# Performance work log

Measured on AMD Instinct MI355X. Metric: run time of the kernel, lower is better.

Reference implementation:

```python
import jax, jax.numpy as jnp
import numpy as np

CHUNKS = 4      # number of segments along in_features
QMAX = 127.0    # int8 symmetric fake quantization
EPS = 1e-8


def fake_quantize(t):
    """Per-tensor symmetric int8 fake quantization with amax scaling (STE-friendly)."""
    amax = jnp.max(jnp.abs(t))
    scale = jnp.maximum(amax / QMAX, EPS)
    q = jnp.clip(jnp.round(t / scale), -QMAX, QMAX) * scale
    # straight-through estimator: identity gradient through the quantizer
    return t + jax.lax.stop_gradient(q - t)


def setup_inputs() -> dict:
    key = jax.random.key(0)
    kx, kw = jax.random.split(key)
    N, K, O = 4096, 4096, 4096  # tokens (B*S), in_features, out_features
    x = jax.random.normal(kx, (N, K), dtype=jnp.float32)
    weight = jax.random.normal(kw, (O, K), dtype=jnp.float32)
    return {"x": x, "weight": weight}


def reference(x, weight):
    # seg_mode='input': split x and weight along in_features into CHUNKS equal chunks,
    # fake-quantize each chunk independently (per-chunk amax scale), run per-chunk
    # GEMMs y_i = fq(x_i) @ fq(w_i)^T and sum over chunks. No bias in 'input' mode.
    N, K = x.shape
    O = weight.shape[0]
    cs = K // CHUNKS
    xc = x.reshape(N, CHUNKS, cs)       # [N, C, cs]
    wc = weight.reshape(O, CHUNKS, cs)  # [O, C, cs]
    fq_chunks = jax.vmap(fake_quantize, in_axes=1, out_axes=1)  # independent amax per chunk
    xq = fq_chunks(xc)
    wq = fq_chunks(wc)
    # sum of per-chunk matmuls == contraction over (chunk, within-chunk) axes
    return jnp.einsum('nck,ock->no', xq, wq)
```

## Files before the change

kernel.cpp:

```cpp
#include <hip/hip_runtime.h>
#include <hip/hip_bf16.h>


constexpr int NDIM = 4096;
constexpr int TOTAL4 = (NDIM * NDIM) / 4;

typedef int i32x4 __attribute__((ext_vector_type(4)));

__global__ __launch_bounds__(256) void amax_kernel(
    const float* __restrict__ x, const float* __restrict__ w,
    unsigned int* __restrict__ amax) {
  const int t = threadIdx.x;
  const int c = blockIdx.x & 3;
  float mx = 0.f, mw = 0.f;
  const float4* x4 = (const float4*)x;
  const float4* w4 = (const float4*)w;
  const int stride = 1024 * 256;
  for (int i = blockIdx.x * 256 + t; i < TOTAL4; i += stride) {
    float4 v = x4[i];
    mx = fmaxf(mx, fmaxf(fmaxf(fabsf(v.x), fabsf(v.y)),
                         fmaxf(fabsf(v.z), fabsf(v.w))));
    float4 u = w4[i];
    mw = fmaxf(mw, fmaxf(fmaxf(fabsf(u.x), fabsf(u.y)),
                         fmaxf(fabsf(u.z), fabsf(u.w))));
  }
  __shared__ float r0[256], r1[256];
  r0[t] = mx; r1[t] = mw;
  __syncthreads();
  for (int off = 128; off; off >>= 1) {
    if (t < off) {
      r0[t] = fmaxf(r0[t], r0[t + off]);
      r1[t] = fmaxf(r1[t], r1[t + off]);
    }
    __syncthreads();
  }
  if (t == 0) {
    atomicMax(&amax[c],     __float_as_uint(r0[0]));
    atomicMax(&amax[4 + c], __float_as_uint(r1[0]));
  }
}

__device__ __forceinline__ signed char quant1(float v, float s) {
  float r = rintf(v / s);
  r = fminf(fmaxf(r, -127.f), 127.f);
  return (signed char)(int)r;
}

__global__ __launch_bounds__(256) void quant_kernel(
    const float* __restrict__ x, const float* __restrict__ w,
    const unsigned int* __restrict__ amax,
    signed char* __restrict__ qx, signed char* __restrict__ qw) {
  const int t = threadIdx.x;
  const int c = blockIdx.x & 3;
  const float sx = fmaxf(__uint_as_float(amax[c])     / 127.0f, 1e-8f);
  const float sw = fmaxf(__uint_as_float(amax[4 + c]) / 127.0f, 1e-8f);
  const float4* x4 = (const float4*)x;
  const float4* w4 = (const float4*)w;
  char4* qx4 = (char4*)qx;
  char4* qw4 = (char4*)qw;
  const int stride = 1024 * 256;
  for (int i = blockIdx.x * 256 + t; i < TOTAL4; i += stride) {
    float4 v = x4[i];
    char4 q;
    q.x = quant1(v.x, sx); q.y = quant1(v.y, sx);
    q.z = quant1(v.z, sx); q.w = quant1(v.w, sx);
    qx4[i] = q;
    float4 u = w4[i];
    char4 p;
    p.x = quant1(u.x, sw); p.y = quant1(u.y, sw);
    p.z = quant1(u.z, sw); p.w = quant1(u.w, sw);
    qw4[i] = p;
  }
}

__device__ __forceinline__ void async16(const void* g, void* l) {
  __builtin_amdgcn_global_load_lds(
      (const __attribute__((address_space(1))) void*)g,
      (__attribute__((address_space(3))) void*)l, 16, 0, 0);
}

__global__ __launch_bounds__(256, 2) void gemm_i8_kernel(
    const signed char* __restrict__ qx, const signed char* __restrict__ qw,
    const unsigned int* __restrict__ amax, float* __restrict__ out) {
  __shared__ __align__(1024) signed char lds_a[2][16384];
  __shared__ __align__(1024) signed char lds_b[2][16384];

  const int t = threadIdx.x;
  const int lane = t & 63;
  const int wave = t >> 6;
  const int brow = blockIdx.y * 128;
  const int bcol = blockIdx.x * 128;
  const int wr = wave >> 1;
  const int wc = wave & 1;

  const float s0 = fmaxf(__uint_as_float(amax[0]) / 127.0f, 1e-8f) *
                   fmaxf(__uint_as_float(amax[4]) / 127.0f, 1e-8f);
  const float s1 = fmaxf(__uint_as_float(amax[1]) / 127.0f, 1e-8f) *
                   fmaxf(__uint_as_float(amax[5]) / 127.0f, 1e-8f);
  const float s2 = fmaxf(__uint_as_float(amax[2]) / 127.0f, 1e-8f) *
                   fmaxf(__uint_as_float(amax[6]) / 127.0f, 1e-8f);
  const float s3 = fmaxf(__uint_as_float(amax[3]) / 127.0f, 1e-8f) *
                   fmaxf(__uint_as_float(amax[7]) / 127.0f, 1e-8f);
  asm volatile("s_waitcnt vmcnt(0)" ::: "memory");
  __builtin_amdgcn_sched_barrier(0);

  const int srow = t >> 3;
  const int scol = (((t & 7) ^ (srow & 7)) << 4);
  const signed char* gA = qx + (size_t)(brow + srow) * NDIM + scol;
  const signed char* gB = qw + (size_t)(bcol + srow) * NDIM + scol;
  signed char* laW = &lds_a[0][0] + wave * 1024;
  signed char* lbW = &lds_b[0][0] + wave * 1024;

  const int kg = lane >> 4;
  const int l7 = lane & 7;
  const int sk0 = ((kg) ^ l7) << 4;
  const int sk1 = ((4 + kg) ^ l7) << 4;
  const int rba = (wr * 64 + (lane & 15)) * 128;
  const int rbb = (wc * 64 + (lane & 15)) * 128;

#define STAGE(BUFOFF, T)                                              \
  do {                                                                \
    const size_t kt_ = (size_t)(T) * 128;                             \
    async16(gA + kt_,                  laW + (BUFOFF));               \
    async16(gA + kt_ + 32u * NDIM,     laW + (BUFOFF) + 4096);        \
    async16(gA + kt_ + 64u * NDIM,     laW + (BUFOFF) + 8192);        \
    async16(gA + kt_ + 96u * NDIM,     laW + (BUFOFF) + 12288);       \
    async16(gB + kt_,                  lbW + (BUFOFF));               \
    async16(gB + kt_ + 32u * NDIM,     lbW + (BUFOFF) + 4096);        \
    async16(gB + kt_ + 64u * NDIM,     lbW + (BUFOFF) + 8192);        \
    async16(gB + kt_ + 96u * NDIM,     lbW + (BUFOFF) + 12288);       \
  } while (0)

  STAGE(0, 0);
  STAGE(16384, 1);

  i32x4 iacc[4][4];
  float facc[4][4][4];
#pragma unroll
  for (int m = 0; m < 4; ++m)
#pragma unroll
    for (int n = 0; n < 4; ++n) {
      iacc[m][n] = i32x4{0, 0, 0, 0};
#pragma unroll
      for (int j = 0; j < 4; ++j) facc[m][n][j] = 0.f;
    }

#define HALF(LA, LB, SK)                                                \
  do {                                                                  \
    i32x4 av[4], bv[4];                                                 \
    _Pragma("unroll")                                                   \
    for (int m = 0; m < 4; ++m)                                         \
      av[m] = *(const i32x4*)&(LA)[rba + m * 2048 + (SK)];              \
    _Pragma("unroll")                                                   \
    for (int n = 0; n < 4; ++n)                                         \
      bv[n] = *(const i32x4*)&(LB)[rbb + n * 2048 + (SK)];              \
    __builtin_amdgcn_s_setprio(1);                                      \
    _Pragma("unroll")                                                   \
    for (int m = 0; m < 4; ++m)                                         \
      _Pragma("unroll")                                                 \
      for (int n = 0; n < 4; ++n)                                       \
        iacc[m][n] = __builtin_amdgcn_mfma_i32_16x16x64_i8(             \
            av[m], bv[n], iacc[m][n], 0, 0, 0);                         \
    __builtin_amdgcn_s_setprio(0);                                      \
  } while (0)

#define COMPUTE(BUFOFF)                                                 \
  do {                                                                  \
    const signed char* la_ = &lds_a[0][0] + (BUFOFF);                   \
    const signed char* lb_ = &lds_b[0][0] + (BUFOFF);                   \
    HALF(la_, lb_, sk0);                                                \
    HALF(la_, lb_, sk1);                                                \
  } while (0)

#define FOLD(S)                                                         \
  do {                                                                  \
    _Pragma("unroll")                                                   \
    for (int m = 0; m < 4; ++m)                                         \
      _Pragma("unroll")                                                 \
      for (int n = 0; n < 4; ++n) {                                     \
        _Pragma("unroll")                                               \
        for (int j = 0; j < 4; ++j) facc[m][n][j] += (S) * (float)iacc[m][n][j]; \
        iacc[m][n] = i32x4{0, 0, 0, 0};                                 \
      }                                                                 \
  } while (0)

#define WAITV(N) \
  asm volatile("s_waitcnt vmcnt(" #N ")" ::: "memory"); \
  __builtin_amdgcn_sched_barrier(0)
#define WAITL \
  asm volatile("s_waitcnt lgkmcnt(0)" ::: "memory"); \
  __builtin_amdgcn_sched_barrier(0)
#define BAR \
  __builtin_amdgcn_s_barrier(); \
  __builtin_amdgcn_sched_barrier(0)

#pragma unroll 1
  for (int it = 0; it < 15; ++it) {
    WAITV(8); BAR;
    COMPUTE(0);
    WAITL; BAR;
    STAGE(0, 2 * it + 2);
    WAITV(8); BAR;
    COMPUTE(16384);
    WAITL; BAR;
    STAGE(16384, 2 * it + 3);
    if ((it & 3) == 3) {
      const int ci = it >> 2;
      FOLD(ci == 0 ? s0 : ci == 1 ? s1 : s2);
    }
  }
  WAITV(8); BAR;
  COMPUTE(0);
  WAITL; BAR;
  WAITV(0); BAR;
  COMPUTE(16384);
  FOLD(s3);

  const int orow = brow + wr * 64 + (lane >> 4) * 4;
  const int ocol = bcol + wc * 64 + (lane & 15);
#pragma unroll
  for (int m = 0; m < 4; ++m)
#pragma unroll
    for (int n = 0; n < 4; ++n)
#pragma unroll
      for (int j = 0; j < 4; ++j)
        out[(size_t)(orow + m * 16 + j) * NDIM + (ocol + n * 16)] = facc[m][n][j];
#undef STAGE
#undef HALF
#undef COMPUTE
#undef FOLD
#undef WAITV
#undef WAITL
#undef BAR
}

extern "C" void kernel_launch(void* const* d_in, const int* in_sizes, int n_in,
                              void* d_out, int out_size, void* d_ws, size_t ws_size,
                              hipStream_t stream) {
  const float* x = (const float*)d_in[0];
  const float* w = (const float*)d_in[1];
  float* out = (float*)d_out;

  unsigned int* amax = (unsigned int*)d_ws;
  signed char* qx = (signed char*)d_ws + 256;
  signed char* qw = qx + (size_t)NDIM * NDIM;

  hipMemsetAsync(d_ws, 0, 256, stream);
  amax_kernel<<<1024, 256, 0, stream>>>(x, w, amax);
  quant_kernel<<<1024, 256, 0, stream>>>(x, w, amax, qx, qw);
  dim3 grid(NDIM / 128, NDIM / 128);
  gemm_i8_kernel<<<grid, 256, 0, stream>>>(qx, qw, amax, out);
}
```

Measured before the change: 144.9 us.

## Load A operand directly to registers and 4-stage B pipeline in LDS

The int8 GEMM stops staging the A tile through LDS. Each wave now loads its A fragments straight from global memory into registers, double-buffered across K steps. The B tile moves to a 4-buffer LDS ring with one barrier per K step instead of two. Occupancy drops to one block per CU, and A rows are no longer shared between the two waves that use them, which doubles A global traffic and raises register pressure.

```diff
diff --git a/kernel.cpp b/kernel.cpp
--- a/kernel.cpp
+++ b/kernel.cpp
@@ -79,11 +79,10 @@
       (__attribute__((address_space(3))) void*)l, 16, 0, 0);
 }
 
-__global__ __launch_bounds__(256, 2) void gemm_i8_kernel(
+__global__ __launch_bounds__(256, 1) void gemm_i8_kernel(
     const signed char* __restrict__ qx, const signed char* __restrict__ qw,
     const unsigned int* __restrict__ amax, float* __restrict__ out) {
-  __shared__ __align__(1024) signed char lds_a[2][16384];
-  __shared__ __align__(1024) signed char lds_b[2][16384];
+  __shared__ __align__(1024) signed char lds_b[4][16384];
 
   const int t = threadIdx.x;
   const int lane = t & 63;
@@ -101,39 +100,54 @@
                    fmaxf(__uint_as_float(amax[6]) / 127.0f, 1e-8f);
   const float s3 = fmaxf(__uint_as_float(amax[3]) / 127.0f, 1e-8f) *
                    fmaxf(__uint_as_float(amax[7]) / 127.0f, 1e-8f);
-  asm volatile("s_waitcnt vmcnt(0)" ::: "memory");
+  asm volatile("s_waitcnt vmcnt(0) lgkmcnt(0)" ::: "memory");
   __builtin_amdgcn_sched_barrier(0);
 
   const int srow = t >> 3;
   const int scol = (((t & 7) ^ (srow & 7)) << 4);
-  const signed char* gA = qx + (size_t)(brow + srow) * NDIM + scol;
   const signed char* gB = qw + (size_t)(bcol + srow) * NDIM + scol;
-  signed char* laW = &lds_a[0][0] + wave * 1024;
-  signed char* lbW = &lds_b[0][0] + wave * 1024;
-
+
+  const int l15 = lane & 15;
   const int kg = lane >> 4;
+  const signed char* gA = qx + (size_t)(brow + wr * 64 + l15) * NDIM + kg * 16;
+
   const int l7 = lane & 7;
   const int sk0 = ((kg) ^ l7) << 4;
   const int sk1 = ((4 + kg) ^ l7) << 4;
-  const int rba = (wr * 64 + (lane & 15)) * 128;
-  const int rbb = (wc * 64 + (lane & 15)) * 128;
-
-#define STAGE(BUFOFF, T)                                              \
+  const int rbb = (wc * 64 + l15) * 128;
+
+#define STAGE_B(BUF, T)                                               \
   do {                                                                \
     const size_t kt_ = (size_t)(T) * 128;                             \
-    async16(gA + kt_,                  laW + (BUFOFF));               \
-    async16(gA + kt_ + 32u * NDIM,     laW + (BUFOFF) + 4096);        \
-    async16(gA + kt_ + 64u * NDIM,     laW + (BUFOFF) + 8192);        \
-    async16(gA + kt_ + 96u * NDIM,     laW + (BUFOFF) + 12288);       \
-    async16(gB + kt_,                  lbW + (BUFOFF));               \
-    async16(gB + kt_ + 32u * NDIM,     lbW + (BUFOFF) + 4096);        \
-    async16(gB + kt_ + 64u * NDIM,     lbW + (BUFOFF) + 8192);        \
-    async16(gB + kt_ + 96u * NDIM,     lbW + (BUFOFF) + 12288);       \
-  } while (0)
-
-  STAGE(0, 0);
-  STAGE(16384, 1);
-
+    async16(gB + kt_,              &lds_b[BUF][0] + t * 16);          \
+    async16(gB + kt_ + 32u * NDIM, &lds_b[BUF][4096] + t * 16);       \
+    async16(gB + kt_ + 64u * NDIM, &lds_b[BUF][8192] + t * 16);       \
+    async16(gB + kt_ + 96u * NDIM, &lds_b[BUF][12288] + t * 16);      \
+  } while (0)
+
+#define LOAD_A(SET, T)                                                \
+  do {                                                                \
+    const size_t kt_ = (size_t)(T) * 128;                             \
+    _Pragma("unroll")                                                 \
+    for (int m = 0; m < 4; ++m)                                       \
+      _Pragma("unroll")                                               \
+      for (int h = 0; h < 2; ++h)                                     \
+        SET[m][h] = *(const i32x4*)(gA + kt_ +                        \
+                                    (size_t)m * (16u * NDIM) + h * 64); \
+  } while (0)
+
+#define MM(AV, BV, M, N) \
+  iacc[M][N] = __builtin_amdgcn_mfma_i32_16x16x64_i8((AV), (BV), iacc[M][N], 0, 0, 0)
+
+#define SCB  __builtin_amdgcn_sched_barrier(0)
+#define WAITV(N) \
+  asm volatile("s_waitcnt vmcnt(" #N ")" ::: "memory"); SCB
+#define WAITL \
+  asm volatile("s_waitcnt lgkmcnt(0)" ::: "memory"); SCB
+#define BAR \
+  __builtin_amdgcn_s_barrier(); SCB
+
+  i32x4 aA[4][2], aB[4][2];
   i32x4 iacc[4][4];
   float facc[4][4][4];
 #pragma unroll
@@ -145,31 +159,27 @@
       for (int j = 0; j < 4; ++j) facc[m][n][j] = 0.f;
     }
 
-#define HALF(LA, LB, SK)                                                \
+  STAGE_B(0, 0); SCB;
+  LOAD_A(aA, 0); SCB;
+  STAGE_B(1, 1); SCB;
+
+#define COMPUTE(BUF, SET)                                               \
   do {                                                                  \
-    i32x4 av[4], bv[4];                                                 \
+    i32x4 bv[4][2];                                                     \
     _Pragma("unroll")                                                   \
-    for (int m = 0; m < 4; ++m)                                         \
-      av[m] = *(const i32x4*)&(LA)[rba + m * 2048 + (SK)];              \
-    _Pragma("unroll")                                                   \
-    for (int n = 0; n < 4; ++n)                                         \
-      bv[n] = *(const i32x4*)&(LB)[rbb + n * 2048 + (SK)];              \
+    for (int n = 0; n < 4; ++n) {                                       \
+      bv[n][0] = *(const i32x4*)&lds_b[BUF][rbb + n * 2048 + sk0];      \
+      bv[n][1] = *(const i32x4*)&lds_b[BUF][rbb + n * 2048 + sk1];      \
+    }                                                                   \
     __builtin_amdgcn_s_setprio(1);                                      \
     _Pragma("unroll")                                                   \
-    for (int m = 0; m < 4; ++m)                                         \
+    for (int h = 0; h < 2; ++h)                                         \
       _Pragma("unroll")                                                 \
-      for (int n = 0; n < 4; ++n)                                       \
-        iacc[m][n] = __builtin_amdgcn_mfma_i32_16x16x64_i8(             \
-            av[m], bv[n], iacc[m][n], 0, 0, 0);                         \
+      for (int m = 0; m < 4; ++m)                                       \
+        _Pragma("unroll")                                               \
+        for (int n = 0; n < 4; ++n)                                     \
+          MM(SET[m][h], bv[n][h], m, n);                                \
     __builtin_amdgcn_s_setprio(0);                                      \
-  } while (0)
-
-#define COMPUTE(BUFOFF)                                                 \
-  do {                                                                  \
-    const signed char* la_ = &lds_a[0][0] + (BUFOFF);                   \
-    const signed char* lb_ = &lds_b[0][0] + (BUFOFF);                   \
-    HALF(la_, lb_, sk0);                                                \
-    HALF(la_, lb_, sk1);                                                \
   } while (0)
 
 #define FOLD(S)                                                         \
@@ -181,43 +191,42 @@
         _Pragma("unroll")                                               \
         for (int j = 0; j < 4; ++j) facc[m][n][j] += (S) * (float)iacc[m][n][j]; \
         iacc[m][n] = i32x4{0, 0, 0, 0};                                 \
-      }                                                                 \
-  } while (0)
-
-#define WAITV(N) \
-  asm volatile("s_waitcnt vmcnt(" #N ")" ::: "memory"); \
-  __builtin_amdgcn_sched_barrier(0)
-#define WAITL \
-  asm volatile("s_waitcnt lgkmcnt(0)" ::: "memory"); \
-  __builtin_amdgcn_sched_barrier(0)
-#define BAR \
-  __builtin_amdgcn_s_barrier(); \
-  __builtin_amdgcn_sched_barrier(0)
+      }                                                                  \
+  } while (0)
+
+#define STEP(P, ST, ASET, ANXT)                                         \
+  do {                                                                  \
+    WAITV(4);                                                           \
+    BAR;                                                                \
+    LOAD_A(ANXT, (ST) + 1); SCB;                                        \
+    STAGE_B(((P) + 2) & 3, (ST) + 2); SCB;                              \
+    COMPUTE(P, ASET);                                                   \
+    WAITL;                                                              \
+  } while (0)
 
 #pragma unroll 1
-  for (int it = 0; it < 15; ++it) {
-    WAITV(8); BAR;
-    COMPUTE(0);
-    WAITL; BAR;
-    STAGE(0, 2 * it + 2);
-    WAITV(8); BAR;
-    COMPUTE(16384);
-    WAITL; BAR;
-    STAGE(16384, 2 * it + 3);
-    if ((it & 3) == 3) {
-      const int ci = it >> 2;
-      FOLD(ci == 0 ? s0 : ci == 1 ? s1 : s2);
-    }
-  }
-  WAITV(8); BAR;
-  COMPUTE(0);
-  WAITL; BAR;
+  for (int k = 0; k < 7; ++k) {
+    const int st = k * 4;
+    STEP(0, st + 0, aA, aB);
+    STEP(1, st + 1, aB, aA);
+    STEP(2, st + 2, aA, aB);
+    STEP(3, st + 3, aB, aA);
+    if (k == 1) FOLD(s0);
+    else if (k == 3) FOLD(s1);
+    else if (k == 5) FOLD(s2);
+  }
+  STEP(0, 28, aA, aB);
+  STEP(1, 29, aB, aA);
+  WAITV(4); BAR;
+  LOAD_A(aB, 31); SCB;
+  COMPUTE(2, aA);
+  WAITL;
   WAITV(0); BAR;
-  COMPUTE(16384);
+  COMPUTE(3, aB);
   FOLD(s3);
 
   const int orow = brow + wr * 64 + (lane >> 4) * 4;
-  const int ocol = bcol + wc * 64 + (lane & 15);
+  const int ocol = bcol + wc * 64 + l15;
 #pragma unroll
   for (int m = 0; m < 4; ++m)
 #pragma unroll
@@ -225,13 +234,16 @@
 #pragma unroll
       for (int j = 0; j < 4; ++j)
         out[(size_t)(orow + m * 16 + j) * NDIM + (ocol + n * 16)] = facc[m][n][j];
-#undef STAGE
-#undef HALF
-#undef COMPUTE
-#undef FOLD
+#undef STAGE_B
+#undef LOAD_A
+#undef MM
+#undef SCB
 #undef WAITV
 #undef WAITL
 #undef BAR
+#undef COMPUTE
+#undef FOLD
+#undef STEP
 }
 
 extern "C" void kernel_launch(void* const* d_in, const int* in_sizes, int n_in,
```

After: 255.5 us. 76.3% more time.
